# Kernel tuning notes

Measured on AMD Instinct MI355X. Metric: run time of the kernel, lower is better.

## Reference

```python
import jax, jax.numpy as jnp
import numpy as np

# BTT dims for in=out=4096, square mode: m=n=64, a=b=64, rank=8
M, N, A, B_BLK, RANK = 64, 64, 64, 64, 8
OUT_FEATURES = M * A  # 4096


def setup_inputs() -> dict:
    key = jax.random.key(0)
    k_x, k_r, k_l = jax.random.split(key, 3)
    x = jax.random.normal(k_x, (4, 1024, 4096), dtype=jnp.float32)
    # btt_r: (n, b, m*rank); btt_l: (m, rank*n, a)
    btt_r = jax.random.normal(k_r, (N, B_BLK, M * RANK), dtype=jnp.float32) * 0.02
    btt_l = jax.random.normal(k_l, (M, RANK * N, A), dtype=jnp.float32) * 0.02
    bias = jnp.zeros((OUT_FEATURES,), dtype=jnp.float32)
    return {"x": x, "btt_r": btt_r, "btt_l": btt_l, "bias": bias}


def reference(x, btt_r, btt_l, bias):
    n, b, mr = btt_r.shape
    m, rn, a = btt_l.shape
    rank = mr // m
    orig_shape = x.shape
    xr = x.reshape(-1, n, b)          # (B, n, b)
    Bn = xr.shape[0]
    # first contraction: bmm over n blocks -> (n, B, m*rank)
    inner = jnp.einsum('Bnb,nbj->nBj', xr, btt_r)
    # reshape/permute exactly as torch: (n,B,m,r) -> (m,B,n,r) -> (m,B,n*r)
    inner = inner.reshape(n, Bn, m, rank).transpose(2, 1, 0, 3).reshape(m, Bn, rank * n)
    # second contraction: bmm over m blocks -> (B, m, a)
    out = jnp.einsum('mBk,mka->Bma', inner, btt_l)
    out = out.reshape(*orig_shape[:-1], m * a)
    return out + bias
```

## Files before the change

kernel.cpp:

```cpp
#include <hip/hip_runtime.h>


typedef float f32x16 __attribute__((ext_vector_type(16)));
typedef short short8 __attribute__((ext_vector_type(8)));

static __device__ __forceinline__ unsigned short f2b(float f) {
    union { float f; unsigned u; } a; a.f = f;
    unsigned u = a.u;
    unsigned r = u + 0x7fffu + ((u >> 16) & 1u);
    return (unsigned short)(r >> 16);
}

static __device__ __forceinline__ void load_lds_16(const void* gptr, void* lptr) {
    __builtin_amdgcn_global_load_lds(
        (const __attribute__((address_space(1))) unsigned int*)gptr,
        (__attribute__((address_space(3))) unsigned int*)lptr, 16, 0, 0);
}

__global__ __launch_bounds__(256) void prep_all(
    const float* __restrict__ x,
    const float* __restrict__ btt_r,
    const float* __restrict__ btt_l,
    unsigned short* __restrict__ xbt,
    unsigned short* __restrict__ Wtt,
    int nx)
{
    const int tid = threadIdx.x;
    if ((int)blockIdx.x < nx) {
        unsigned i = blockIdx.x * 256 + tid;
        int row = ((i >> 12) << 3) | (i & 7);
        int g   = (i >> 3) & 511;
        float4 v0 = *(const float4*)(x + (size_t)row * 4096 + g * 8);
        float4 v1 = *(const float4*)(x + (size_t)row * 4096 + g * 8 + 4);
        unsigned short o[8];
        o[0] = f2b(v0.x); o[1] = f2b(v0.y); o[2] = f2b(v0.z); o[3] = f2b(v0.w);
        o[4] = f2b(v1.x); o[5] = f2b(v1.y); o[6] = f2b(v1.z); o[7] = f2b(v1.w);
        int ks = g >> 1, half = g & 1;
        int rt = row >> 8, rb = (row >> 5) & 7, l31 = row & 31;
        size_t dst = ((((size_t)rt * 256 + ks) * 8 + rb) * 64 + half * 32 + l31) * 8;
        *(uint4*)(xbt + dst) = *(const uint4*)o;
        return;
    }
    __shared__ float Rs[64][8];
    __shared__ float Ls[8][64];
    const int wb = blockIdx.x - nx;
    const int m = wb >> 6, n = wb & 63;

    if (tid < 128) {
        int b = tid >> 1, rh = (tid & 1) * 4;
        float4 v = *(const float4*)(btt_r + (size_t)n * 32768 + (size_t)b * 512 + m * 8 + rh);
        *(float4*)&Rs[b][rh] = v;
    } else {
        int t2 = (tid - 128) * 4;
        float4 v = *(const float4*)(btt_l + (size_t)m * 32768 + n * 512 + t2);
        *(float4*)&(&Ls[0][0])[t2] = v;
    }
    __syncthreads();

    const int a  = tid >> 2;
    const int bg = (tid & 3) * 16;
    float la[8];
    #pragma unroll
    for (int r = 0; r < 8; ++r) la[r] = Ls[r][a];

    unsigned short o[16];
    #pragma unroll
    for (int bb = 0; bb < 16; ++bb) {
        float acc = 0.f;
        #pragma unroll
        for (int r = 0; r < 8; ++r) acc += Rs[bg + bb][r] * la[r];
        o[bb] = f2b(acc);
    }
    int col = m * 64 + a;
    int ct = col >> 8, rb = (col >> 5) & 7, l31 = col & 31;
    int ks = n * 4 + (bg >> 4);
    size_t dst = ((((size_t)ct * 256 + ks) * 8 + rb) * 64 + l31) * 8;
    *(uint4*)(Wtt + dst)           = *(const uint4*)&o[0];
    *(uint4*)(Wtt + dst + 32 * 8)  = *(const uint4*)&o[8];
}

__global__ __launch_bounds__(512, 2) void gemm_btt(
    const unsigned short* __restrict__ xbt,
    const unsigned short* __restrict__ Wtt,
    const float* __restrict__ bias,
    float* __restrict__ out)
{
    __shared__ unsigned short As[8][4096];
    __shared__ unsigned short Bs[8][4096];

    const int tid = threadIdx.x;
    const int bid = blockIdx.x;
    const int jj = bid >> 3, xc = bid & 7;
    const int rt = (xc >> 1) * 4 + (jj >> 3);
    const int ct = (xc & 1) * 8 + (jj & 7);

    const int wid = tid >> 6, l = tid & 63;
    const int l31 = l & 31, half = l >> 5;
    const int wr = wid >> 2;
    const int wc = wid & 3;

    const unsigned short* xa = xbt + (size_t)rt * (256 * 4096);
    const unsigned short* wa = Wtt + (size_t)ct * (256 * 4096);

    const int offA0 = ((wr * 4 + 0) * 64 + l) * 8;
    const int offA1 = ((wr * 4 + 1) * 64 + l) * 8;
    const int offA2 = ((wr * 4 + 2) * 64 + l) * 8;
    const int offA3 = ((wr * 4 + 3) * 64 + l) * 8;
    const int offB0 = ((wc * 2 + 0) * 64 + l) * 8;
    const int offB1 = ((wc * 2 + 1) * 64 + l) * 8;

    f32x16 acc[4][2];
    #pragma unroll
    for (int i = 0; i < 4; ++i)
        #pragma unroll
        for (int j = 0; j < 2; ++j)
            #pragma unroll
            for (int r = 0; r < 16; ++r)
                acc[i][j][r] = 0.f;

    short8 fA0, fA1, fA2, fA3, fB0, fB1;
    short8 gA0, gA1, gA2, gA3, gB0, gB1;

    #define STAGE(s, slot) do {                                               \
        load_lds_16(xa + (size_t)(s) * 4096 + tid * 8, &As[slot][tid * 8]);   \
        load_lds_16(wa + (size_t)(s) * 4096 + tid * 8, &Bs[slot][tid * 8]);   \
    } while (0)

    #define READ6(pA0,pA1,pA2,pA3,pB0,pB1, slot) do {                         \
        const unsigned short* Ab = &As[slot][0];                              \
        const unsigned short* Bb = &Bs[slot][0];                              \
        pA0 = *(const short8*)(Ab + offA0);                                   \
        pA1 = *(const short8*)(Ab + offA1);                                   \
        pA2 = *(const short8*)(Ab + offA2);                                   \
        pA3 = *(const short8*)(Ab + offA3);                                   \
        pB0 = *(const short8*)(Bb + offB0);                                   \
        pB1 = *(const short8*)(Bb + offB1);                                   \
    } while (0)

    #define MFMA8(cA0,cA1,cA2,cA3,cB0,cB1) do {                               \
        __builtin_amdgcn_s_setprio(1);                                        \
        acc[0][0] = __builtin_amdgcn_mfma_f32_32x32x16_bf16(cA0, cB0, acc[0][0], 0, 0, 0); \
        acc[0][1] = __builtin_amdgcn_mfma_f32_32x32x16_bf16(cA0, cB1, acc[0][1], 0, 0, 0); \
        acc[1][0] = __builtin_amdgcn_mfma_f32_32x32x16_bf16(cA1, cB0, acc[1][0], 0, 0, 0); \
        acc[1][1] = __builtin_amdgcn_mfma_f32_32x32x16_bf16(cA1, cB1, acc[1][1], 0, 0, 0); \
        acc[2][0] = __builtin_amdgcn_mfma_f32_32x32x16_bf16(cA2, cB0, acc[2][0], 0, 0, 0); \
        acc[2][1] = __builtin_amdgcn_mfma_f32_32x32x16_bf16(cA2, cB1, acc[2][1], 0, 0, 0); \
        acc[3][0] = __builtin_amdgcn_mfma_f32_32x32x16_bf16(cA3, cB0, acc[3][0], 0, 0, 0); \
        acc[3][1] = __builtin_amdgcn_mfma_f32_32x32x16_bf16(cA3, cB1, acc[3][1], 0, 0, 0); \
        __builtin_amdgcn_s_setprio(0);                                        \
    } while (0)

    #define PHASE(STAGE_STMT, VMSTR, rslot, pA0,pA1,pA2,pA3,pB0,pB1, cA0,cA1,cA2,cA3,cB0,cB1) do { \
        STAGE_STMT;                                                           \
        asm volatile(VMSTR ::: "memory");                                     \
        __builtin_amdgcn_s_barrier();                                         \
        asm volatile("" ::: "memory");                                        \
        READ6(pA0,pA1,pA2,pA3,pB0,pB1, rslot);                                \
        MFMA8(cA0,cA1,cA2,cA3,cB0,cB1);                                       \
    } while (0)

    STAGE(0, 0); STAGE(1, 1); STAGE(2, 2); STAGE(3, 3);
    asm volatile("s_waitcnt vmcnt(6)" ::: "memory");
    __builtin_amdgcn_s_barrier();
    asm volatile("" ::: "memory");
    READ6(fA0, fA1, fA2, fA3, fB0, fB1, 0);

    #pragma unroll 1
    for (int it = 0; it < 31; ++it) {
        const int s0 = it * 8;
        PHASE(STAGE(s0 + 4,  4), "s_waitcnt vmcnt(6)", 1, gA0,gA1,gA2,gA3,gB0,gB1, fA0,fA1,fA2,fA3,fB0,fB1);
        PHASE(STAGE(s0 + 5,  5), "s_waitcnt vmcnt(6)", 2, fA0,fA1,fA2,fA3,fB0,fB1, gA0,gA1,gA2,gA3,gB0,gB1);
        PHASE(STAGE(s0 + 6,  6), "s_waitcnt vmcnt(6)", 3, gA0,gA1,gA2,gA3,gB0,gB1, fA0,fA1,fA2,fA3,fB0,fB1);
        PHASE(STAGE(s0 + 7,  7), "s_waitcnt vmcnt(6)", 4, fA0,fA1,fA2,fA3,fB0,fB1, gA0,gA1,gA2,gA3,gB0,gB1);
        PHASE(STAGE(s0 + 8,  0), "s_waitcnt vmcnt(6)", 5, gA0,gA1,gA2,gA3,gB0,gB1, fA0,fA1,fA2,fA3,fB0,fB1);
        PHASE(STAGE(s0 + 9,  1), "s_waitcnt vmcnt(6)", 6, fA0,fA1,fA2,fA3,fB0,fB1, gA0,gA1,gA2,gA3,gB0,gB1);
        PHASE(STAGE(s0 + 10, 2), "s_waitcnt vmcnt(6)", 7, gA0,gA1,gA2,gA3,gB0,gB1, fA0,fA1,fA2,fA3,fB0,fB1);
        PHASE(STAGE(s0 + 11, 3), "s_waitcnt vmcnt(6)", 0, fA0,fA1,fA2,fA3,fB0,fB1, gA0,gA1,gA2,gA3,gB0,gB1);
    }
    PHASE(STAGE(252, 4), "s_waitcnt vmcnt(6)", 1, gA0,gA1,gA2,gA3,gB0,gB1, fA0,fA1,fA2,fA3,fB0,fB1);
    PHASE(STAGE(253, 5), "s_waitcnt vmcnt(6)", 2, fA0,fA1,fA2,fA3,fB0,fB1, gA0,gA1,gA2,gA3,gB0,gB1);
    PHASE(STAGE(254, 6), "s_waitcnt vmcnt(6)", 3, gA0,gA1,gA2,gA3,gB0,gB1, fA0,fA1,fA2,fA3,fB0,fB1);
    PHASE(STAGE(255, 7), "s_waitcnt vmcnt(6)", 4, fA0,fA1,fA2,fA3,fB0,fB1, gA0,gA1,gA2,gA3,gB0,gB1);
    PHASE(((void)0),     "s_waitcnt vmcnt(4)", 5, gA0,gA1,gA2,gA3,gB0,gB1, fA0,fA1,fA2,fA3,fB0,fB1);
    PHASE(((void)0),     "s_waitcnt vmcnt(2)", 6, fA0,fA1,fA2,fA3,fB0,fB1, gA0,gA1,gA2,gA3,gB0,gB1);
    PHASE(((void)0),     "s_waitcnt vmcnt(0)", 7, gA0,gA1,gA2,gA3,gB0,gB1, fA0,fA1,fA2,fA3,fB0,fB1);
    MFMA8(gA0, gA1, gA2, gA3, gB0, gB1);

    const int rowTileBase = rt * 256 + wr * 128;
    const int colTileBase = ct * 256 + wc * 64;
    #pragma unroll
    for (int jn = 0; jn < 2; ++jn) {
        const int col = colTileBase + jn * 32 + l31;
        const float bv = bias[col];
        #pragma unroll
        for (int i = 0; i < 4; ++i) {
            const int rbase = rowTileBase + i * 32 + 4 * half;
            #pragma unroll
            for (int r = 0; r < 16; ++r) {
                int row = rbase + (r & 3) + 8 * (r >> 2);
                out[(size_t)row * 4096 + col] = acc[i][jn][r] + bv;
            }
        }
    }
    #undef STAGE
    #undef READ6
    #undef MFMA8
    #undef PHASE
}

extern "C" void kernel_launch(void* const* d_in, const int* in_sizes, int n_in,
                              void* d_out, int out_size, void* d_ws, size_t ws_size,
                              hipStream_t stream) {
    const float* x    = (const float*)d_in[0];
    const float* r    = (const float*)d_in[1];
    const float* l    = (const float*)d_in[2];
    const float* bias = (const float*)d_in[3];
    float* out = (float*)d_out;

    unsigned short* xbt = (unsigned short*)d_ws;
    unsigned short* Wtt = (unsigned short*)d_ws + (size_t)4096 * 4096;

    const int rows = in_sizes[0] / 4096;
    const int nx = rows * 4096 / 8 / 256;

    prep_all<<<dim3(nx + 4096), dim3(256), 0, stream>>>(x, r, l, xbt, Wtt, nx);
    gemm_btt<<<dim3((rows / 256) * 16), dim3(512), 0, stream>>>(xbt, Wtt, bias, out);
}
```

Before: 280.5 us.

## Process two K-stages per barrier with deeper six-stage LDS prefetch

The main GEMM loop now handles two K-slices per barrier instead of one, halving the number of s_barrier synchronisations. It prefetches six stages ahead instead of four and issues the next loads after the barrier rather than before. Both slices' fragments are read from LDS up front, followed by sixteen MFMAs under raised priority. The trade-offs are no overlap of LDS reads with the previous MFMAs, higher register pressure from holding both fragment sets, and a changed slot-reuse pattern that depends on the barrier placement for correctness.

Measured after the change: 278.6 us. Within noise of the previous version (-0.7%).

```diff
diff --git a/kernel.cpp b/kernel.cpp
--- a/kernel.cpp
+++ b/kernel.cpp
@@ -126,6 +126,13 @@
         load_lds_16(wa + (size_t)(s) * 4096 + tid * 8, &Bs[slot][tid * 8]);   \
     } while (0)
 
+    #define STAGE2(sa, sla, sb, slb) do {                                     \
+        STAGE(sa, sla);                                                       \
+        STAGE(sb, slb);                                                       \
+    } while (0)
+
+    #define NOSTAGE do { } while (0)
+
     #define READ6(pA0,pA1,pA2,pA3,pB0,pB1, slot) do {                         \
         const unsigned short* Ab = &As[slot][0];                              \
         const unsigned short* Bb = &Bs[slot][0];                              \
@@ -138,7 +145,6 @@
     } while (0)
 
     #define MFMA8(cA0,cA1,cA2,cA3,cB0,cB1) do {                               \
-        __builtin_amdgcn_s_setprio(1);                                        \
         acc[0][0] = __builtin_amdgcn_mfma_f32_32x32x16_bf16(cA0, cB0, acc[0][0], 0, 0, 0); \
         acc[0][1] = __builtin_amdgcn_mfma_f32_32x32x16_bf16(cA0, cB1, acc[0][1], 0, 0, 0); \
         acc[1][0] = __builtin_amdgcn_mfma_f32_32x32x16_bf16(cA1, cB0, acc[1][0], 0, 0, 0); \
@@ -147,44 +153,35 @@
         acc[2][1] = __builtin_amdgcn_mfma_f32_32x32x16_bf16(cA2, cB1, acc[2][1], 0, 0, 0); \
         acc[3][0] = __builtin_amdgcn_mfma_f32_32x32x16_bf16(cA3, cB0, acc[3][0], 0, 0, 0); \
         acc[3][1] = __builtin_amdgcn_mfma_f32_32x32x16_bf16(cA3, cB1, acc[3][1], 0, 0, 0); \
-        __builtin_amdgcn_s_setprio(0);                                        \
-    } while (0)
-
-    #define PHASE(STAGE_STMT, VMSTR, rslot, pA0,pA1,pA2,pA3,pB0,pB1, cA0,cA1,cA2,cA3,cB0,cB1) do { \
-        STAGE_STMT;                                                           \
+    } while (0)
+
+    #define SUPER(e, STAGE_STMT, VMSTR) do {                                  \
         asm volatile(VMSTR ::: "memory");                                     \
         __builtin_amdgcn_s_barrier();                                         \
         asm volatile("" ::: "memory");                                        \
-        READ6(pA0,pA1,pA2,pA3,pB0,pB1, rslot);                                \
-        MFMA8(cA0,cA1,cA2,cA3,cB0,cB1);                                       \
-    } while (0)
-
-    STAGE(0, 0); STAGE(1, 1); STAGE(2, 2); STAGE(3, 3);
-    asm volatile("s_waitcnt vmcnt(6)" ::: "memory");
-    __builtin_amdgcn_s_barrier();
-    asm volatile("" ::: "memory");
-    READ6(fA0, fA1, fA2, fA3, fB0, fB1, 0);
+        STAGE_STMT;                                                           \
+        READ6(fA0,fA1,fA2,fA3,fB0,fB1, (e));                                  \
+        READ6(gA0,gA1,gA2,gA3,gB0,gB1, (e) + 1);                              \
+        __builtin_amdgcn_s_setprio(1);                                        \
+        MFMA8(fA0,fA1,fA2,fA3,fB0,fB1);                                       \
+        MFMA8(gA0,gA1,gA2,gA3,gB0,gB1);                                       \
+        __builtin_amdgcn_s_setprio(0);                                        \
+    } while (0)
+
+    STAGE(0, 0); STAGE(1, 1); STAGE(2, 2); STAGE(3, 3); STAGE(4, 4); STAGE(5, 5);
 
     #pragma unroll 1
-    for (int it = 0; it < 31; ++it) {
-        const int s0 = it * 8;
-        PHASE(STAGE(s0 + 4,  4), "s_waitcnt vmcnt(6)", 1, gA0,gA1,gA2,gA3,gB0,gB1, fA0,fA1,fA2,fA3,fB0,fB1);
-        PHASE(STAGE(s0 + 5,  5), "s_waitcnt vmcnt(6)", 2, fA0,fA1,fA2,fA3,fB0,fB1, gA0,gA1,gA2,gA3,gB0,gB1);
-        PHASE(STAGE(s0 + 6,  6), "s_waitcnt vmcnt(6)", 3, gA0,gA1,gA2,gA3,gB0,gB1, fA0,fA1,fA2,fA3,fB0,fB1);
-        PHASE(STAGE(s0 + 7,  7), "s_waitcnt vmcnt(6)", 4, fA0,fA1,fA2,fA3,fB0,fB1, gA0,gA1,gA2,gA3,gB0,gB1);
-        PHASE(STAGE(s0 + 8,  0), "s_waitcnt vmcnt(6)", 5, gA0,gA1,gA2,gA3,gB0,gB1, fA0,fA1,fA2,fA3,fB0,fB1);
-        PHASE(STAGE(s0 + 9,  1), "s_waitcnt vmcnt(6)", 6, fA0,fA1,fA2,fA3,fB0,fB1, gA0,gA1,gA2,gA3,gB0,gB1);
-        PHASE(STAGE(s0 + 10, 2), "s_waitcnt vmcnt(6)", 7, gA0,gA1,gA2,gA3,gB0,gB1, fA0,fA1,fA2,fA3,fB0,fB1);
-        PHASE(STAGE(s0 + 11, 3), "s_waitcnt vmcnt(6)", 0, fA0,fA1,fA2,fA3,fB0,fB1, gA0,gA1,gA2,gA3,gB0,gB1);
-    }
-    PHASE(STAGE(252, 4), "s_waitcnt vmcnt(6)", 1, gA0,gA1,gA2,gA3,gB0,gB1, fA0,fA1,fA2,fA3,fB0,fB1);
-    PHASE(STAGE(253, 5), "s_waitcnt vmcnt(6)", 2, fA0,fA1,fA2,fA3,fB0,fB1, gA0,gA1,gA2,gA3,gB0,gB1);
-    PHASE(STAGE(254, 6), "s_waitcnt vmcnt(6)", 3, gA0,gA1,gA2,gA3,gB0,gB1, fA0,fA1,fA2,fA3,fB0,fB1);
-    PHASE(STAGE(255, 7), "s_waitcnt vmcnt(6)", 4, fA0,fA1,fA2,fA3,fB0,fB1, gA0,gA1,gA2,gA3,gB0,gB1);
-    PHASE(((void)0),     "s_waitcnt vmcnt(4)", 5, gA0,gA1,gA2,gA3,gB0,gB1, fA0,fA1,fA2,fA3,fB0,fB1);
-    PHASE(((void)0),     "s_waitcnt vmcnt(2)", 6, fA0,fA1,fA2,fA3,fB0,fB1, gA0,gA1,gA2,gA3,gB0,gB1);
-    PHASE(((void)0),     "s_waitcnt vmcnt(0)", 7, gA0,gA1,gA2,gA3,gB0,gB1, fA0,fA1,fA2,fA3,fB0,fB1);
-    MFMA8(gA0, gA1, gA2, gA3, gB0, gB1);
+    for (int it2 = 0; it2 < 31; ++it2) {
+        const int s8 = it2 * 8;
+        SUPER(0, STAGE2(s8 + 6,  6, s8 + 7,  7), "s_waitcnt vmcnt(8)");
+        SUPER(2, STAGE2(s8 + 8,  0, s8 + 9,  1), "s_waitcnt vmcnt(8)");
+        SUPER(4, STAGE2(s8 + 10, 2, s8 + 11, 3), "s_waitcnt vmcnt(8)");
+        SUPER(6, STAGE2(s8 + 12, 4, s8 + 13, 5), "s_waitcnt vmcnt(8)");
+    }
+    SUPER(0, STAGE2(254, 6, 255, 7), "s_waitcnt vmcnt(8)");
+    SUPER(2, NOSTAGE,                "s_waitcnt vmcnt(8)");
+    SUPER(4, NOSTAGE,                "s_waitcnt vmcnt(4)");
+    SUPER(6, NOSTAGE,                "s_waitcnt vmcnt(0)");
 
     const int rowTileBase = rt * 256 + wr * 128;
     const int colTileBase = ct * 256 + wc * 64;
@@ -203,9 +200,11 @@
         }
     }
     #undef STAGE
+    #undef STAGE2
+    #undef NOSTAGE
     #undef READ6
     #undef MFMA8
-    #undef PHASE
+    #undef SUPER
 }
 
 extern "C" void kernel_launch(void* const* d_in, const int* in_sizes, int n_in,
```
